# Optimization experiments

Measured on AMD Instinct MI355X. Metric: run time of the kernel, lower is better.

Reference implementation:

```python
import jax, jax.numpy as jnp
import numpy as np

EPS_LN = 1e-5
EPS_BN = 1e-5


def ln_channels(x, w, b):
    # LayerNorm2d: normalize over channel dim of NCHW
    mu = x.mean(axis=1, keepdims=True)
    var = x.var(axis=1, keepdims=True)
    return (x - mu) / jnp.sqrt(var + EPS_LN) * w[None, :, None, None] + b[None, :, None, None]


def bn_eval(x, g, b):
    # eval-mode BatchNorm2d with running_mean=0, running_var=1
    return x / jnp.sqrt(1.0 + EPS_BN) * g[None, :, None, None] + b[None, :, None, None]


def conv1x1(x, w, b):
    return jnp.einsum('bchw,oc->bohw', x, w) + b[None, :, None, None]


def q_shift(x):
    # directional shift: 4 channel quarters shifted right/left/down/up by 1 px (zero pad)
    C = x.shape[1]
    q = C // 4
    return jnp.concatenate([
        jnp.pad(x[:, 0 * q:1 * q, :, :-1], ((0, 0), (0, 0), (0, 0), (1, 0))),
        jnp.pad(x[:, 1 * q:2 * q, :, 1:], ((0, 0), (0, 0), (0, 0), (0, 1))),
        jnp.pad(x[:, 2 * q:3 * q, :-1, :], ((0, 0), (0, 0), (1, 0), (0, 0))),
        jnp.pad(x[:, 3 * q:4 * q, 1:, :], ((0, 0), (0, 0), (0, 1), (0, 0))),
    ], axis=1)


def wkv_scan(k, v, w_neg, u):
    # numerically-stable RWKV WKV recurrence. k, v: [N, T, C]; w_neg (negative decay), u: [C]
    N, T, C = k.shape

    def step(carry, kv):
        a, b, p = carry
        kt, vt = kv
        q = jnp.maximum(p, u + kt)
        e1 = jnp.exp(p - q)
        e2 = jnp.exp(u + kt - q)
        out = (e1 * a + e2 * vt) / (e1 * b + e2)
        q2 = jnp.maximum(p + w_neg, kt)
        f1 = jnp.exp(p + w_neg - q2)
        f2 = jnp.exp(kt - q2)
        return (f1 * a + f2 * vt, f1 * b + f2, q2), out

    init = (jnp.zeros((N, C), k.dtype), jnp.zeros((N, C), k.dtype), jnp.full((N, C), -1e38, k.dtype))
    _, outs = jax.lax.scan(step, init, (jnp.swapaxes(k, 0, 1), jnp.swapaxes(v, 0, 1)))
    return jnp.swapaxes(outs, 0, 1)


def shape_guided_rwkv(x, mask, mix_k, mix_v, mix_r, Wk, Wv, Wr, Wo, decay, first, kn_w, kn_b):
    B, C, H, W = x.shape
    xs = q_shift(x)
    x_sh = mask * xs + (1.0 - mask) * x  # saliency-guided shift blend
    mk = mix_k[None, :, None, None]
    mv = mix_v[None, :, None, None]
    mr = mix_r[None, :, None, None]
    xk = x * mk + x_sh * (1.0 - mk)
    xv = x * mv + x_sh * (1.0 - mv)
    xr = x * mr + x_sh * (1.0 - mr)
    k = jnp.einsum('bchw,oc->bohw', xk, Wk)
    v = jnp.einsum('bchw,oc->bohw', xv, Wv)
    sr = jax.nn.sigmoid(jnp.einsum('bchw,oc->bohw', xr, Wr))
    w_neg = -jnp.exp(decay)
    # horizontal orientation: scan each row left->right
    kh = k.transpose(0, 2, 3, 1).reshape(B * H, W, C)
    vh = v.transpose(0, 2, 3, 1).reshape(B * H, W, C)
    wkv_h = wkv_scan(kh, vh, w_neg, first).reshape(B, H, W, C).transpose(0, 3, 1, 2)
    # vertical orientation: scan each column top->bottom
    kv_ = k.transpose(0, 3, 2, 1).reshape(B * W, H, C)
    vv_ = v.transpose(0, 3, 2, 1).reshape(B * W, H, C)
    wkv_v = wkv_scan(kv_, vv_, w_neg, first).reshape(B, W, H, C).transpose(0, 3, 2, 1)
    wkv = 0.5 * (wkv_h + wkv_v)
    wkv = ln_channels(wkv, kn_w, kn_b)  # key_norm=True
    out = jnp.einsum('bchw,oc->bohw', sr * wkv, Wo)
    return x + out


def channel_fusion(x, c1_w, c1_b, bn1_g, bn1_b, c2_w, c2_b, bn2_g, bn2_b, c3_w, c3_b, bn3_g, bn3_b):
    # grouped 3x3 conv (groups=2) -> GELU -> BN -> 1x1 expand -> GELU -> BN -> 1x1 reduce -> GELU -> BN
    y = jax.lax.conv_general_dilated(x, c1_w, (1, 1), 'SAME',
                                     dimension_numbers=('NCHW', 'OIHW', 'NCHW'),
                                     feature_group_count=2) + c1_b[None, :, None, None]
    y = bn_eval(jax.nn.gelu(y, approximate=False), bn1_g, bn1_b)
    y = bn_eval(jax.nn.gelu(conv1x1(y, c2_w, c2_b), approximate=False), bn2_g, bn2_b)
    y = bn_eval(jax.nn.gelu(conv1x1(y, c3_w, c3_b), approximate=False), bn3_g, bn3_b)
    return y


def patch_expand(x, up_w, up_b, s=2):
    B, C, H, W = x.shape
    y = conv1x1(x, up_w, up_b)  # [B, Cout*s*s, H, W]
    Cout = y.shape[1] // (s * s)
    y = y.reshape(B, Cout, s, s, H, W).transpose(0, 1, 4, 2, 5, 3).reshape(B, Cout, H * s, W * s)
    return y


def setup_inputs() -> dict:
    key = jax.random.key(0)
    B, C, Cs, Cout, H, W, s = 8, 256, 512, 128, 64, 64, 2
    ks = jax.random.split(key, 32)
    sc = C ** -0.5
    inp = {
        'x': jax.random.normal(ks[0], (B, C, H, W), jnp.float32),
        'skip': jax.random.normal(ks[1], (B, Cs, H, W), jnp.float32),
        'saliency_mask': jax.random.uniform(ks[2], (B, 1, H, W), jnp.float32),
        'ln1_w': jnp.ones((C,)), 'ln1_b': jnp.zeros((C,)),
        'ln2_w': jnp.ones((C,)), 'ln2_b': jnp.zeros((C,)),
        'mix_k': jax.random.uniform(ks[3], (C,)),
        'mix_v': jax.random.uniform(ks[4], (C,)),
        'mix_r': jax.random.uniform(ks[5], (C,)),
        'Wk': jax.random.normal(ks[6], (C, C)) * sc,
        'Wv': jax.random.normal(ks[7], (C, C)) * sc,
        'Wr': jax.random.normal(ks[8], (C, C)) * sc,
        'Wo': jax.random.normal(ks[9], (C, C)) * sc,
        'decay': jax.random.normal(ks[10], (C,)) * 0.5,
        'first': jax.random.normal(ks[11], (C,)) * 0.5,
        'kn_w': jnp.ones((C,)), 'kn_b': jnp.zeros((C,)),
        'sp_w': jax.random.normal(ks[12], (C, Cs)) * (Cs ** -0.5),
        'sp_b': jnp.zeros((C,)),
        'c1_w': jax.random.normal(ks[13], (2 * C, C, 3, 3)) * ((C * 9) ** -0.5),
        'c1_b': jnp.zeros((2 * C,)),
        'bn1_g': jnp.ones((2 * C,)), 'bn1_b': jnp.zeros((2 * C,)),
        'c2_w': jax.random.normal(ks[14], (4 * C, 2 * C)) * ((2 * C) ** -0.5),
        'c2_b': jnp.zeros((4 * C,)),
        'bn2_g': jnp.ones((4 * C,)), 'bn2_b': jnp.zeros((4 * C,)),
        'c3_w': jax.random.normal(ks[15], (C, 4 * C)) * ((4 * C) ** -0.5),
        'c3_b': jnp.zeros((C,)),
        'bn3_g': jnp.ones((C,)), 'bn3_b': jnp.zeros((C,)),
        'up_w': jax.random.normal(ks[16], (Cout * s * s, C)) * sc,
        'up_b': jnp.zeros((Cout * s * s,)),
    }
    return inp


def reference(x, skip, saliency_mask, ln1_w, ln1_b, ln2_w, ln2_b, mix_k, mix_v, mix_r,
              Wk, Wv, Wr, Wo, decay, first, kn_w, kn_b, sp_w, sp_b,
              c1_w, c1_b, bn1_g, bn1_b, c2_w, c2_b, bn2_g, bn2_b, c3_w, c3_b, bn3_g, bn3_b,
              up_w, up_b):
    xn = ln_channels(x, ln1_w, ln1_b)
    x_sg = shape_guided_rwkv(xn, saliency_mask, mix_k, mix_v, mix_r, Wk, Wv, Wr, Wo,
                             decay, first, kn_w, kn_b)
    skip_feat = conv1x1(skip, sp_w, sp_b)
    x_cat = jnp.concatenate([x_sg, skip_feat], axis=1)
    x_fused = channel_fusion(x_cat, c1_w, c1_b, bn1_g, bn1_b, c2_w, c2_b, bn2_g, bn2_b,
                             c3_w, c3_b, bn3_g, bn3_b)
    x_fused = ln_channels(x_fused, ln2_w, ln2_b)
    return patch_expand(x_fused, up_w, up_b, s=2)
```

## Files before the change

### kernel.cpp

```cpp
#include <hip/hip_runtime.h>
#include <hip/hip_bf16.h>
#include <math.h>

#define B_ 8
#define C_ 256
#define P_ 4096

typedef __bf16 bf16_t;
typedef __attribute__((ext_vector_type(8))) __bf16 bf16x8;
typedef __attribute__((ext_vector_type(4))) float f32x4;

__global__ __launch_bounds__(256)
void ln_stats_kernel(const float* __restrict__ in, float2* __restrict__ stats)
{
    __shared__ float sred[4][64];
    __shared__ float s2red[4][64];
    int tid = threadIdx.x;
    int wp = tid & 63, cw = tid >> 6;
    int gp = blockIdx.x * 64 + wp;
    int b  = gp >> 12, p = gp & 4095;
    size_t base = (size_t)b * 256 * 4096 + p;
    float s = 0.f, s2 = 0.f;
    #pragma unroll 8
    for (int cc = 0; cc < 64; ++cc) {
        float v = in[base + (size_t)(cw * 64 + cc) * 4096];
        s += v; s2 += v * v;
    }
    sred[cw][wp] = s; s2red[cw][wp] = s2;
    __syncthreads();
    if (cw == 0) {
        s  = sred[0][wp]  + sred[1][wp]  + sred[2][wp]  + sred[3][wp];
        s2 = s2red[0][wp] + s2red[1][wp] + s2red[2][wp] + s2red[3][wp];
        float mu  = s * (1.f / 256.f);
        float var = s2 * (1.f / 256.f) - mu * mu;
        stats[gp] = make_float2(mu, 1.0f / sqrtf(var + 1e-5f));
    }
}

__global__ __launch_bounds__(256)
void qshift_mix_kernel(const float* __restrict__ x, const float2* __restrict__ st1,
                       const float* __restrict__ mask,
                       const float* __restrict__ gw, const float* __restrict__ gb,
                       const float* __restrict__ mk_, const float* __restrict__ mv_,
                       const float* __restrict__ mr_,
                       bf16_t* __restrict__ xk, bf16_t* __restrict__ xv,
                       bf16_t* __restrict__ xr)
{
    int g = blockIdx.x * 256 + threadIdx.x;
    int p = g & 4095;
    int c = (g >> 12) & 255;
    int b = g >> 20;
    int h = p >> 6, w = p & 63;
    float gwc = gw[c], gbc = gb[c];
    float2 stc = st1[(b << 12) + p];
    float xcv = (x[g] - stc.x) * stc.y * gwc + gbc;
    float xs = 0.f;
    int quad = c >> 6;
    int d = 0; bool ok = false;
    if (quad == 0)      { ok = (w > 0);  d = -1;  }
    else if (quad == 1) { ok = (w < 63); d = 1;   }
    else if (quad == 2) { ok = (h > 0);  d = -64; }
    else                { ok = (h < 63); d = 64;  }
    if (ok) {
        float2 st2 = st1[(b << 12) + p + d];
        xs = (x[g + d] - st2.x) * st2.y * gwc + gbc;
    }
    float m = mask[(b << 12) + p];
    float xsh = m * xs + (1.f - m) * xcv;
    float a;
    a = mk_[c]; xk[g] = (bf16_t)(a * xcv + (1.f - a) * xsh);
    a = mv_[c]; xv[g] = (bf16_t)(a * xcv + (1.f - a) * xsh);
    a = mr_[c]; xr[g] = (bf16_t)(a * xcv + (1.f - a) * xsh);
}

#define EP_NONE    0
#define EP_SIGMOID 1
#define EP_BIAS    2
#define EP_RESLN   3
#define EP_GELU_BN 4
#define EP_SHUFFLE 5

template<int NB, int BMODE, int EPI, int OUTBF>
__global__ __launch_bounds__(256)
void mfma_gemm(const bf16_t* __restrict__ Wp, const void* __restrict__ Xin,
               const float* __restrict__ X2,
               const float2* __restrict__ bstats, const float* __restrict__ blnw,
               const float* __restrict__ blnb,
               const float* __restrict__ bias, const float* __restrict__ bng,
               const float* __restrict__ bnb,
               const float* __restrict__ resx, const float2* __restrict__ estats,
               const float* __restrict__ elnw, const float* __restrict__ elnb,
               void* __restrict__ OutV,
               int O, int K, int Cstride, int obs, int ocoff)
{
    __shared__ bf16_t Alds[NB * 128 * 40];
    __shared__ bf16_t Blds[66 * 40];
    int tid = threadIdx.x;
    int bx = blockIdx.x;
    int o0 = blockIdx.y * 128;
    int b  = blockIdx.z;
    int p0 = bx << 6;
    int cbase = (NB == 3) ? ((o0 >> 8) << 8) : 0;

    int lane = tid & 63, wid = tid >> 6;
    int l15 = lane & 15;
    int lk8 = (lane >> 4) << 3;
    int mbase = (wid >> 1) << 6;
    int nbase = (wid & 1) << 5;

    int wl = lane;
    int cg = wid;
    int ao = tid >> 1, aq = tid & 1;

    const bf16_t* Xb_bf = (const bf16_t*)Xin + (size_t)b * Cstride * 4096;
    const float*  Xb_f  = (const float*)Xin + (size_t)b * Cstride * 4096;
    const float*  X2b   = (BMODE == 3) ? X2 + (size_t)b * Cstride * 4096 : nullptr;

    f32x4 acc[4][2] = {};

    if (tid < 40) { Blds[tid] = (bf16_t)0.f; Blds[65 * 40 + tid] = (bf16_t)0.f; }

    for (int kh = 0; kh < NB; ++kh) {
        bool rowok = true;
        int srcp = p0;
        if (NB == 3) {
            int hh = bx + kh - 1;
            rowok = (hh >= 0) && (hh < 64);
            srcp = hh << 6;
        }
        for (int c0 = 0; c0 < K; c0 += 32) {
            __syncthreads();
            bf16x8 bv;
            #pragma unroll
            for (int i = 0; i < 8; ++i) bv[i] = (bf16_t)0.f;
            if (rowok) {
                size_t gbase = (size_t)(cbase + c0 + cg * 8) * 4096 + srcp + wl;
                float2 st = make_float2(0.f, 0.f);
                if (BMODE >= 2) st = bstats[(b << 12) + srcp + wl];
                #pragma unroll
                for (int j = 0; j < 8; ++j) {
                    size_t gi = gbase + (size_t)j * 4096;
                    int cc = c0 + cg * 8 + j;
                    if (BMODE == 0)      bv[j] = Xb_bf[gi];
                    else if (BMODE == 1) bv[j] = (bf16_t)Xb_f[gi];
                    else {
                        float v = (Xb_f[gi] - st.x) * st.y * blnw[cc] + blnb[cc];
                        if (BMODE == 3) v *= X2b[gi];
                        bv[j] = (bf16_t)v;
                    }
                }
            }
            *reinterpret_cast<bf16x8*>(&Blds[(wl + 1) * 40 + cg * 8]) = bv;
            #pragma unroll
            for (int t = 0; t < NB; ++t) {
                const bf16_t* wsrc = (NB == 3)
                    ? Wp + ((size_t)(kh * 3 + t) * O + o0 + ao) * 256 + c0
                    : Wp + (size_t)(o0 + ao) * K + c0;
                bf16x8 w0 = *reinterpret_cast<const bf16x8*>(wsrc + aq * 8);
                bf16x8 w1 = *reinterpret_cast<const bf16x8*>(wsrc + (aq + 2) * 8);
                *reinterpret_cast<bf16x8*>(&Alds[t * 5120 + ao * 40 + aq * 8]) = w0;
                *reinterpret_cast<bf16x8*>(&Alds[t * 5120 + ao * 40 + (aq + 2) * 8]) = w1;
            }
            __syncthreads();
            #pragma unroll
            for (int t = 0; t < NB; ++t) {
                int kws = (NB == 3) ? t : 1;
                bf16x8 af[4], bfv[2];
                #pragma unroll
                for (int i = 0; i < 4; ++i)
                    af[i] = *reinterpret_cast<const bf16x8*>(
                              &Alds[t * 5120 + (mbase + i * 16 + l15) * 40 + lk8]);
                #pragma unroll
                for (int j = 0; j < 2; ++j)
                    bfv[j] = *reinterpret_cast<const bf16x8*>(
                              &Blds[(nbase + j * 16 + l15 + kws) * 40 + lk8]);
                #pragma unroll
                for (int i = 0; i < 4; ++i)
                    #pragma unroll
                    for (int j = 0; j < 2; ++j)
                        acc[i][j] = __builtin_amdgcn_mfma_f32_16x16x32_bf16(
                                        af[i], bfv[j], acc[i][j], 0, 0, 0);
            }
        }
    }

    const float bnsc = 1.0f / sqrtf(1.f + 1e-5f);
    #pragma unroll
    for (int i = 0; i < 4; ++i) {
        #pragma unroll
        for (int r = 0; r < 4; ++r) {
            int o = o0 + mbase + i * 16 + ((lane >> 4) << 2) + r;
            float bi = (EPI == EP_BIAS || EPI == EP_GELU_BN || EPI == EP_SHUFFLE)
                       ? bias[o] : 0.f;
            float sc = 0.f, sh = 0.f;
            if (EPI == EP_GELU_BN) { sc = bng[o] * bnsc; sh = bnb[o]; }
            float rw = 0.f, rb = 0.f;
            if (EPI == EP_RESLN) { rw = elnw[o]; rb = elnb[o]; }
            #pragma unroll
            for (int j = 0; j < 2; ++j) {
                int pp = p0 + nbase + j * 16 + l15;
                float t = acc[i][j][r];
                if (EPI == EP_SIGMOID) t = 1.f / (1.f + expf(-t));
                if (EPI == EP_BIAS || EPI == EP_GELU_BN || EPI == EP_SHUFFLE) t += bi;
                if (EPI == EP_RESLN) {
                    float2 st = estats[(b << 12) + pp];
                    float rv = resx[((size_t)b * 256 + o) * 4096 + pp];
                    t += (rv - st.x) * st.y * rw + rb;
                }
                if (EPI == EP_GELU_BN) {
                    t = 0.5f * t * (1.f + erff(t * 0.70710678118654752f));
                    t = t * sc + sh;
                }
                if (EPI == EP_SHUFFLE) {
                    int co = o >> 2, s1 = (o >> 1) & 1, s2 = o & 1;
                    int hh = pp >> 6, ww = pp & 63;
                    ((float*)OutV)[(((size_t)b * 128 + co) * 128 + hh * 2 + s1) * 128
                                   + ww * 2 + s2] = t;
                } else {
                    size_t oidx = ((size_t)b * obs + ocoff + o) * 4096 + pp;
                    if (OUTBF) ((bf16_t*)OutV)[oidx] = (bf16_t)t;
                    else       ((float*)OutV)[oidx]  = t;
                }
            }
        }
    }
}

__global__ __launch_bounds__(256)
void repack_conv_w(const float* __restrict__ w, bf16_t* __restrict__ out)
{
    int g = blockIdx.x * 256 + threadIdx.x;
    int c = g & 255;
    int o = (g >> 8) & 511;
    int tap = g >> 17;
    out[g] = (bf16_t)w[(size_t)o * 2304 + c * 9 + tap];
}

__global__ __launch_bounds__(256)
void pack_weights(const float* __restrict__ wk, const float* __restrict__ wv,
                  const float* __restrict__ wr, const float* __restrict__ wo,
                  const float* __restrict__ sp, const float* __restrict__ c2,
                  const float* __restrict__ c3, const float* __restrict__ up,
                  bf16_t* __restrict__ out)
{
    int g = blockIdx.x * 256 + threadIdx.x;
    float v;
    if      (g < 65536)   v = wk[g];
    else if (g < 131072)  v = wv[g - 65536];
    else if (g < 196608)  v = wr[g - 131072];
    else if (g < 262144)  v = wo[g - 196608];
    else if (g < 393216)  v = sp[g - 262144];
    else if (g < 917504)  v = c2[g - 393216];
    else if (g < 1179648) v = c3[g - 917504];
    else                  v = up[g - 1179648];
    out[g] = (bf16_t)v;
}

__global__ __launch_bounds__(64)
void wkv_h_kernel(const float* __restrict__ kin, const float* __restrict__ vin,
                  float* __restrict__ outw,
                  const float* __restrict__ decay, const float* __restrict__ first)
{
    __shared__ float ks[64][65];
    __shared__ float vs[64][65];
    int c0 = blockIdx.x * 64;
    int h  = blockIdx.y;
    int b  = blockIdx.z;
    int tid = threadIdx.x;
    size_t base = (((size_t)b * 256 + c0) * 64 + h) * 64;

    for (int f = tid; f < 64 * 64; f += 64) {
        int cc = f >> 6, w = f & 63;
        ks[cc][w] = kin[base + (size_t)cc * 4096 + w];
        vs[cc][w] = vin[base + (size_t)cc * 4096 + w];
    }
    __syncthreads();

    int c = c0 + tid;
    float u  = first[c];
    float wn = -expf(decay[c]);
    float a = 0.f, bb = 0.f, pp = -1e38f;
    for (int t = 0; t < 64; ++t) {
        float kt = ks[tid][t], vt = vs[tid][t];
        float q  = fmaxf(pp, u + kt);
        float e1 = expf(pp - q), e2 = expf(u + kt - q);
        float ov = (e1 * a + e2 * vt) / (e1 * bb + e2);
        ks[tid][t] = ov;
        float q2 = fmaxf(pp + wn, kt);
        float f1 = expf(pp + wn - q2), f2 = expf(kt - q2);
        a = f1 * a + f2 * vt;
        bb = f1 * bb + f2;
        pp = q2;
    }
    __syncthreads();
    for (int f = tid; f < 64 * 64; f += 64) {
        int cc = f >> 6, w = f & 63;
        outw[base + (size_t)cc * 4096 + w] = ks[cc][w];
    }
}

__global__ __launch_bounds__(256)
void wkv_v_kernel(const float* __restrict__ kin, const float* __restrict__ vin,
                  float* __restrict__ outw,
                  const float* __restrict__ decay, const float* __restrict__ first)
{
    int g = blockIdx.x * 256 + threadIdx.x;
    int w = g & 63;
    int c = (g >> 6) & 255;
    int b = g >> 14;
    size_t base = (size_t)(b * 256 + c) * 4096 + w;
    float u  = first[c];
    float wn = -expf(decay[c]);
    float a = 0.f, bb = 0.f, pp = -1e38f;
    for (int h = 0; h < 64; ++h) {
        size_t idx = base + h * 64;
        float kt = kin[idx], vt = vin[idx];
        float q  = fmaxf(pp, u + kt);
        float e1 = expf(pp - q), e2 = expf(u + kt - q);
        float ov = (e1 * a + e2 * vt) / (e1 * bb + e2);
        outw[idx] = 0.5f * (outw[idx] + ov);
        float q2 = fmaxf(pp + wn, kt);
        float f1 = expf(pp + wn - q2), f2 = expf(kt - q2);
        a = f1 * a + f2 * vt;
        bb = f1 * bb + f2;
        pp = q2;
    }
}

extern "C" void kernel_launch(void* const* d_in, const int* in_sizes, int n_in,
                              void* d_out, int out_size, void* d_ws, size_t ws_size,
                              hipStream_t stream)
{
    const float* x      = (const float*)d_in[0];
    const float* skip   = (const float*)d_in[1];
    const float* mask   = (const float*)d_in[2];
    const float* ln1_w  = (const float*)d_in[3];
    const float* ln1_b  = (const float*)d_in[4];
    const float* ln2_w  = (const float*)d_in[5];
    const float* ln2_b  = (const float*)d_in[6];
    const float* mix_k  = (const float*)d_in[7];
    const float* mix_v  = (const float*)d_in[8];
    const float* mix_r  = (const float*)d_in[9];
    const float* Wk     = (const float*)d_in[10];
    const float* Wv     = (const float*)d_in[11];
    const float* Wr     = (const float*)d_in[12];
    const float* Wo     = (const float*)d_in[13];
    const float* decay  = (const float*)d_in[14];
    const float* first  = (const float*)d_in[15];
    const float* kn_w   = (const float*)d_in[16];
    const float* kn_b   = (const float*)d_in[17];
    const float* sp_w   = (const float*)d_in[18];
    const float* sp_b   = (const float*)d_in[19];
    const float* c1_w   = (const float*)d_in[20];
    const float* c1_b   = (const float*)d_in[21];
    const float* bn1_g  = (const float*)d_in[22];
    const float* bn1_b  = (const float*)d_in[23];
    const float* c2_w   = (const float*)d_in[24];
    const float* c2_b   = (const float*)d_in[25];
    const float* bn2_g  = (const float*)d_in[26];
    const float* bn2_b  = (const float*)d_in[27];
    const float* c3_w   = (const float*)d_in[28];
    const float* c3_b   = (const float*)d_in[29];
    const float* bn3_g  = (const float*)d_in[30];
    const float* bn3_b  = (const float*)d_in[31];
    const float* up_w   = (const float*)d_in[32];
    const float* up_b   = (const float*)d_in[33];
    float* out = (float*)d_out;

    float* ws = (float*)d_ws;
    const size_t S = 8388608;
    bf16_t* xk   = (bf16_t*)ws;
    bf16_t* xv   = (bf16_t*)(ws + S / 2);
    bf16_t* xr   = (bf16_t*)(ws + S);
    float*  kbuf = ws + 3 * S / 2;
    float*  vbuf = ws + 5 * S / 2;
    float*  rbuf = ws + 7 * S / 2;
    float*  wkv  = ws;
    bf16_t* xcat = (bf16_t*)(ws + 3 * S / 2);
    bf16_t* y1   = (bf16_t*)(ws + 5 * S / 2);
    bf16_t* y2   = (bf16_t*)ws;
    float*  y3   = ws + 2 * S;
    float*  wtop = ws + 9 * S / 2;
    bf16_t* w9   = (bf16_t*)wtop;
    bf16_t* wfl  = w9 + 1179648;
    float2* st1  = (float2*)(wfl + 1310720);
    float2* stk  = st1 + 32768;
    float2* st2  = stk + 32768;
    bf16_t* wkb = wfl;
    bf16_t* wvb = wfl + 65536;
    bf16_t* wrb = wfl + 131072;
    bf16_t* wob = wfl + 196608;
    bf16_t* spb = wfl + 262144;
    bf16_t* c2b = wfl + 393216;
    bf16_t* c3b = wfl + 917504;
    bf16_t* upb = wfl + 1179648;

    dim3 blk(256);

    pack_weights<<<dim3(5120), blk, 0, stream>>>(Wk, Wv, Wr, Wo, sp_w, c2_w, c3_w, up_w, wfl);
    repack_conv_w<<<dim3(4608), blk, 0, stream>>>(c1_w, w9);
    ln_stats_kernel<<<dim3(512), blk, 0, stream>>>(x, st1);

    qshift_mix_kernel<<<dim3(32768), blk, 0, stream>>>(x, st1, mask, ln1_w, ln1_b,
                                                       mix_k, mix_v, mix_r, xk, xv, xr);
    mfma_gemm<1, 0, EP_NONE, 0><<<dim3(64, 2, 8), blk, 0, stream>>>(
        wkb, xk, nullptr, nullptr, nullptr, nullptr, nullptr, nullptr, nullptr,
        nullptr, nullptr, nullptr, nullptr, kbuf, 256, 256, 256, 256, 0);
    mfma_gemm<1, 0, EP_NONE, 0><<<dim3(64, 2, 8), blk, 0, stream>>>(
        wvb, xv, nullptr, nullptr, nullptr, nullptr, nullptr, nullptr, nullptr,
        nullptr, nullptr, nullptr, nullptr, vbuf, 256, 256, 256, 256, 0);
    mfma_gemm<1, 0, EP_SIGMOID, 0><<<dim3(64, 2, 8), blk, 0, stream>>>(
        wrb, xr, nullptr, nullptr, nullptr, nullptr, nullptr, nullptr, nullptr,
        nullptr, nullptr, nullptr, nullptr, rbuf, 256, 256, 256, 256, 0);
    wkv_h_kernel<<<dim3(4, 64, 8), dim3(64), 0, stream>>>(kbuf, vbuf, wkv, decay, first);
    wkv_v_kernel<<<dim3(512), blk, 0, stream>>>(kbuf, vbuf, wkv, decay, first);
    ln_stats_kernel<<<dim3(512), blk, 0, stream>>>(wkv, stk);
    mfma_gemm<1, 3, EP_RESLN, 1><<<dim3(64, 2, 8), blk, 0, stream>>>(
        wob, wkv, rbuf, stk, kn_w, kn_b, nullptr, nullptr, nullptr,
        x, st1, ln1_w, ln1_b, xcat, 256, 256, 256, 512, 0);
    mfma_gemm<1, 1, EP_BIAS, 1><<<dim3(64, 2, 8), blk, 0, stream>>>(
        spb, skip, nullptr, nullptr, nullptr, nullptr, sp_b, nullptr, nullptr,
        nullptr, nullptr, nullptr, nullptr, xcat, 256, 512, 512, 512, 256);
    mfma_gemm<3, 0, EP_GELU_BN, 1><<<dim3(64, 4, 8), blk, 0, stream>>>(
        w9, xcat, nullptr, nullptr, nullptr, nullptr, c1_b, bn1_g, bn1_b,
        nullptr, nullptr, nullptr, nullptr, y1, 512, 256, 512, 512, 0);
    mfma_gemm<1, 0, EP_GELU_BN, 1><<<dim3(64, 8, 8), blk, 0, stream>>>(
        c2b, y1, nullptr, nullptr, nullptr, nullptr, c2_b, bn2_g, bn2_b,
        nullptr, nullptr, nullptr, nullptr, y2, 1024, 512, 512, 1024, 0);
    mfma_gemm<1, 0, EP_GELU_BN, 0><<<dim3(64, 2, 8), blk, 0, stream>>>(
        c3b, y2, nullptr, nullptr, nullptr, nullptr, c3_b, bn3_g, bn3_b,
        nullptr, nullptr, nullptr, nullptr, y3, 256, 1024, 1024, 256, 0);
    ln_stats_kernel<<<dim3(512), blk, 0, stream>>>(y3, st2);
    mfma_gemm<1, 2, EP_SHUFFLE, 0><<<dim3(64, 4, 8), blk, 0, stream>>>(
        upb, y3, nullptr, st2, ln2_w, ln2_b, up_b, nullptr, nullptr,
        nullptr, nullptr, nullptr, nullptr, out, 512, 256, 256, 0, 0);
}
```

Baseline: 527.8 us.

## Double GEMM pixel tile to 128 columns with two-row conv halo and tighter LDS padding

The MFMA GEMM now computes a 128x128 output tile per block instead of 128x64. Each wave holds a 4x4 accumulator array and the B operand is staged as 128 pixels, or two 66-wide image rows for the 3x3 conv. This aims to raise weight reuse per block, halving A-tile global loads per output, and to raise the MFMA-to-load ratio. The LDS row pitch shrinks from 40 to 36 elements and launch bounds request two blocks per CU. The cost is more registers per thread and half as many blocks, which lowers parallelism on a large-CU GPU and may change LDS bank conflicts.

```diff
diff --git a/kernel.cpp b/kernel.cpp
--- a/kernel.cpp
+++ b/kernel.cpp
@@ -81,7 +81,7 @@
 #define EP_SHUFFLE 5
 
 template<int NB, int BMODE, int EPI, int OUTBF>
-__global__ __launch_bounds__(256)
+__global__ __launch_bounds__(256, 2)
 void mfma_gemm(const bf16_t* __restrict__ Wp, const void* __restrict__ Xin,
                const float* __restrict__ X2,
                const float2* __restrict__ bstats, const float* __restrict__ blnw,
@@ -93,93 +93,111 @@
                void* __restrict__ OutV,
                int O, int K, int Cstride, int obs, int ocoff)
 {
-    __shared__ bf16_t Alds[NB * 128 * 40];
-    __shared__ bf16_t Blds[66 * 40];
+    constexpr int BROWS = (NB == 3) ? 2 * 66 : 128;
+    __shared__ bf16_t Alds[NB * 128 * 36];
+    __shared__ bf16_t Blds[BROWS * 36];
     int tid = threadIdx.x;
     int bx = blockIdx.x;
     int o0 = blockIdx.y * 128;
     int b  = blockIdx.z;
-    int p0 = bx << 6;
+    int p0 = bx << 7;
     int cbase = (NB == 3) ? ((o0 >> 8) << 8) : 0;
 
     int lane = tid & 63, wid = tid >> 6;
     int l15 = lane & 15;
     int lk8 = (lane >> 4) << 3;
     int mbase = (wid >> 1) << 6;
-    int nbase = (wid & 1) << 5;
-
-    int wl = lane;
-    int cg = wid;
-    int ao = tid >> 1, aq = tid & 1;
+    int nbase = (wid & 1) << 6;
 
     const bf16_t* Xb_bf = (const bf16_t*)Xin + (size_t)b * Cstride * 4096;
     const float*  Xb_f  = (const float*)Xin + (size_t)b * Cstride * 4096;
     const float*  X2b   = (BMODE == 3) ? X2 + (size_t)b * Cstride * 4096 : nullptr;
 
-    f32x4 acc[4][2] = {};
-
-    if (tid < 40) { Blds[tid] = (bf16_t)0.f; Blds[65 * 40 + tid] = (bf16_t)0.f; }
+    f32x4 acc[4][4] = {};
+
+    if (NB == 3 && tid < 144) {
+        int r = tid / 72, rest = tid % 72;
+        int col = rest / 36, cc = rest % 36;
+        Blds[(r * 66 + (col ? 65 : 0)) * 36 + cc] = (bf16_t)0.f;
+    }
 
     for (int kh = 0; kh < NB; ++kh) {
-        bool rowok = true;
-        int srcp = p0;
-        if (NB == 3) {
-            int hh = bx + kh - 1;
-            rowok = (hh >= 0) && (hh < 64);
-            srcp = hh << 6;
-        }
         for (int c0 = 0; c0 < K; c0 += 32) {
             __syncthreads();
-            bf16x8 bv;
-            #pragma unroll
-            for (int i = 0; i < 8; ++i) bv[i] = (bf16_t)0.f;
-            if (rowok) {
-                size_t gbase = (size_t)(cbase + c0 + cg * 8) * 4096 + srcp + wl;
-                float2 st = make_float2(0.f, 0.f);
-                if (BMODE >= 2) st = bstats[(b << 12) + srcp + wl];
+            if (NB == 3) {
+                int wpos = tid & 63, cgr = tid >> 6;
                 #pragma unroll
-                for (int j = 0; j < 8; ++j) {
-                    size_t gi = gbase + (size_t)j * 4096;
-                    int cc = c0 + cg * 8 + j;
-                    if (BMODE == 0)      bv[j] = Xb_bf[gi];
-                    else if (BMODE == 1) bv[j] = (bf16_t)Xb_f[gi];
-                    else {
-                        float v = (Xb_f[gi] - st.x) * st.y * blnw[cc] + blnb[cc];
-                        if (BMODE == 3) v *= X2b[gi];
-                        bv[j] = (bf16_t)v;
+                for (int r = 0; r < 2; ++r) {
+                    int hr = (bx << 1) + kh - 1 + r;
+                    bf16x8 bv;
+                    #pragma unroll
+                    for (int i = 0; i < 8; ++i) bv[i] = (bf16_t)0.f;
+                    if (hr >= 0 && hr < 64) {
+                        size_t gb = (size_t)(cbase + c0 + cgr * 8) * 4096 + (hr << 6) + wpos;
+                        #pragma unroll
+                        for (int j = 0; j < 8; ++j) bv[j] = Xb_bf[gb + (size_t)j * 4096];
                     }
+                    *reinterpret_cast<bf16x8*>(&Blds[(r * 66 + wpos + 1) * 36 + cgr * 8]) = bv;
+                }
+            } else {
+                #pragma unroll
+                for (int rep = 0; rep < 2; ++rep) {
+                    int p_loc = tid & 127;
+                    int cgr = (tid >> 7) + rep * 2;
+                    bf16x8 bv;
+                    size_t gbase = (size_t)(c0 + cgr * 8) * 4096 + p0 + p_loc;
+                    float2 st = make_float2(0.f, 1.f);
+                    if (BMODE >= 2) st = bstats[(b << 12) + p0 + p_loc];
+                    #pragma unroll
+                    for (int j = 0; j < 8; ++j) {
+                        size_t gi = gbase + (size_t)j * 4096;
+                        int cc = c0 + cgr * 8 + j;
+                        if (BMODE == 0)      bv[j] = Xb_bf[gi];
+                        else if (BMODE == 1) bv[j] = (bf16_t)Xb_f[gi];
+                        else {
+                            float v = (Xb_f[gi] - st.x) * st.y * blnw[cc] + blnb[cc];
+                            if (BMODE == 3) v *= X2b[gi];
+                            bv[j] = (bf16_t)v;
+                        }
+                    }
+                    *reinterpret_cast<bf16x8*>(&Blds[p_loc * 36 + cgr * 8]) = bv;
                 }
             }
-            *reinterpret_cast<bf16x8*>(&Blds[(wl + 1) * 40 + cg * 8]) = bv;
-            #pragma unroll
-            for (int t = 0; t < NB; ++t) {
-                const bf16_t* wsrc = (NB == 3)
-                    ? Wp + ((size_t)(kh * 3 + t) * O + o0 + ao) * 256 + c0
-                    : Wp + (size_t)(o0 + ao) * K + c0;
-                bf16x8 w0 = *reinterpret_cast<const bf16x8*>(wsrc + aq * 8);
-                bf16x8 w1 = *reinterpret_cast<const bf16x8*>(wsrc + (aq + 2) * 8);
-                *reinterpret_cast<bf16x8*>(&Alds[t * 5120 + ao * 40 + aq * 8]) = w0;
-                *reinterpret_cast<bf16x8*>(&Alds[t * 5120 + ao * 40 + (aq + 2) * 8]) = w1;
+            {
+                int ao = tid >> 1, aq = tid & 1;
+                #pragma unroll
+                for (int t = 0; t < NB; ++t) {
+                    const bf16_t* wsrc = (NB == 3)
+                        ? Wp + ((size_t)(kh * 3 + t) * O + o0 + ao) * 256 + c0
+                        : Wp + (size_t)(o0 + ao) * K + c0;
+                    bf16x8 w0 = *reinterpret_cast<const bf16x8*>(wsrc + aq * 8);
+                    bf16x8 w1 = *reinterpret_cast<const bf16x8*>(wsrc + (aq + 2) * 8);
+                    *reinterpret_cast<bf16x8*>(&Alds[(t * 128 + ao) * 36 + aq * 8]) = w0;
+                    *reinterpret_cast<bf16x8*>(&Alds[(t * 128 + ao) * 36 + (aq + 2) * 8]) = w1;
+                }
             }
             __syncthreads();
             #pragma unroll
             for (int t = 0; t < NB; ++t) {
-                int kws = (NB == 3) ? t : 1;
-                bf16x8 af[4], bfv[2];
+                bf16x8 af[4];
                 #pragma unroll
                 for (int i = 0; i < 4; ++i)
                     af[i] = *reinterpret_cast<const bf16x8*>(
-                              &Alds[t * 5120 + (mbase + i * 16 + l15) * 40 + lk8]);
+                              &Alds[(t * 128 + mbase + i * 16 + l15) * 36 + lk8]);
                 #pragma unroll
-                for (int j = 0; j < 2; ++j)
-                    bfv[j] = *reinterpret_cast<const bf16x8*>(
-                              &Blds[(nbase + j * 16 + l15 + kws) * 40 + lk8]);
-                #pragma unroll
-                for (int i = 0; i < 4; ++i)
+                for (int j = 0; j < 4; ++j) {
+                    int pl = nbase + j * 16;
+                    int baddr;
+                    if (NB == 3)
+                        baddr = ((pl >> 6) * 66 + (pl & 63) + l15 + t) * 36 + lk8;
+                    else
+                        baddr = (pl + l15) * 36 + lk8;
+                    bf16x8 bfv = *reinterpret_cast<const bf16x8*>(&Blds[baddr]);
                     #pragma unroll
-                    for (int j = 0; j < 2; ++j)
+                    for (int i = 0; i < 4; ++i)
                         acc[i][j] = __builtin_amdgcn_mfma_f32_16x16x32_bf16(
-                                        af[i], bfv[j], acc[i][j], 0, 0, 0);
+                                        af[i], bfv, acc[i][j], 0, 0, 0);
+                }
             }
         }
     }
@@ -197,7 +215,7 @@
             float rw = 0.f, rb = 0.f;
             if (EPI == EP_RESLN) { rw = elnw[o]; rb = elnb[o]; }
             #pragma unroll
-            for (int j = 0; j < 2; ++j) {
+            for (int j = 0; j < 4; ++j) {
                 int pp = p0 + nbase + j * 16 + l15;
                 float t = acc[i][j][r];
                 if (EPI == EP_SIGMOID) t = 1.f / (1.f + expf(-t));
@@ -403,35 +421,35 @@
 
     qshift_mix_kernel<<<dim3(32768), blk, 0, stream>>>(x, st1, mask, ln1_w, ln1_b,
                                                        mix_k, mix_v, mix_r, xk, xv, xr);
-    mfma_gemm<1, 0, EP_NONE, 0><<<dim3(64, 2, 8), blk, 0, stream>>>(
+    mfma_gemm<1, 0, EP_NONE, 0><<<dim3(32, 2, 8), blk, 0, stream>>>(
         wkb, xk, nullptr, nullptr, nullptr, nullptr, nullptr, nullptr, nullptr,
         nullptr, nullptr, nullptr, nullptr, kbuf, 256, 256, 256, 256, 0);
-    mfma_gemm<1, 0, EP_NONE, 0><<<dim3(64, 2, 8), blk, 0, stream>>>(
+    mfma_gemm<1, 0, EP_NONE, 0><<<dim3(32, 2, 8), blk, 0, stream>>>(
         wvb, xv, nullptr, nullptr, nullptr, nullptr, nullptr, nullptr, nullptr,
         nullptr, nullptr, nullptr, nullptr, vbuf, 256, 256, 256, 256, 0);
-    mfma_gemm<1, 0, EP_SIGMOID, 0><<<dim3(64, 2, 8), blk, 0, stream>>>(
+    mfma_gemm<1, 0, EP_SIGMOID, 0><<<dim3(32, 2, 8), blk, 0, stream>>>(
         wrb, xr, nullptr, nullptr, nullptr, nullptr, nullptr, nullptr, nullptr,
         nullptr, nullptr, nullptr, nullptr, rbuf, 256, 256, 256, 256, 0);
     wkv_h_kernel<<<dim3(4, 64, 8), dim3(64), 0, stream>>>(kbuf, vbuf, wkv, decay, first);
     wkv_v_kernel<<<dim3(512), blk, 0, stream>>>(kbuf, vbuf, wkv, decay, first);
     ln_stats_kernel<<<dim3(512), blk, 0, stream>>>(wkv, stk);
-    mfma_gemm<1, 3, EP_RESLN, 1><<<dim3(64, 2, 8), blk, 0, stream>>>(
+    mfma_gemm<1, 3, EP_RESLN, 1><<<dim3(32, 2, 8), blk, 0, stream>>>(
         wob, wkv, rbuf, stk, kn_w, kn_b, nullptr, nullptr, nullptr,
         x, st1, ln1_w, ln1_b, xcat, 256, 256, 256, 512, 0);
-    mfma_gemm<1, 1, EP_BIAS, 1><<<dim3(64, 2, 8), blk, 0, stream>>>(
+    mfma_gemm<1, 1, EP_BIAS, 1><<<dim3(32, 2, 8), blk, 0, stream>>>(
         spb, skip, nullptr, nullptr, nullptr, nullptr, sp_b, nullptr, nullptr,
         nullptr, nullptr, nullptr, nullptr, xcat, 256, 512, 512, 512, 256);
-    mfma_gemm<3, 0, EP_GELU_BN, 1><<<dim3(64, 4, 8), blk, 0, stream>>>(
+    mfma_gemm<3, 0, EP_GELU_BN, 1><<<dim3(32, 4, 8), blk, 0, stream>>>(
         w9, xcat, nullptr, nullptr, nullptr, nullptr, c1_b, bn1_g, bn1_b,
         nullptr, nullptr, nullptr, nullptr, y1, 512, 256, 512, 512, 0);
-    mfma_gemm<1, 0, EP_GELU_BN, 1><<<dim3(64, 8, 8), blk, 0, stream>>>(
+    mfma_gemm<1, 0, EP_GELU_BN, 1><<<dim3(32, 8, 8), blk, 0, stream>>>(
         c2b, y1, nullptr, nullptr, nullptr, nullptr, c2_b, bn2_g, bn2_b,
         nullptr, nullptr, nullptr, nullptr, y2, 1024, 512, 512, 1024, 0);
-    mfma_gemm<1, 0, EP_GELU_BN, 0><<<dim3(64, 2, 8), blk, 0, stream>>>(
+    mfma_gemm<1, 0, EP_GELU_BN, 0><<<dim3(32, 2, 8), blk, 0, stream>>>(
         c3b, y2, nullptr, nullptr, nullptr, nullptr, c3_b, bn3_g, bn3_b,
         nullptr, nullptr, nullptr, nullptr, y3, 256, 1024, 1024, 256, 0);
     ln_stats_kernel<<<dim3(512), blk, 0, stream>>>(y3, st2);
-    mfma_gemm<1, 2, EP_SHUFFLE, 0><<<dim3(64, 4, 8), blk, 0, stream>>>(
+    mfma_gemm<1, 2, EP_SHUFFLE, 0><<<dim3(32, 4, 8), blk, 0, stream>>>(
         upb, y3, nullptr, st2, ln2_w, ln2_b, up_b, nullptr, nullptr,
         nullptr, nullptr, nullptr, nullptr, out, 512, 256, 256, 0, 0);
 }
```

New measurement: 506.7 us. -4.0%, faster.
